# Kernel optimization log

Hardware: AMD Instinct MI355X
Metric: run time of the kernel (lower is better)

Reference implementation:

```python
import jax, jax.numpy as jnp
import numpy as np

D_MODEL = 512
NEG = -1e9


def setup_inputs() -> dict:
    key = jax.random.key(0)
    ks = jax.random.split(key, 8)
    B, S, D = 8, 2048, D_MODEL
    scale = 1.0 / np.sqrt(D)
    x = jax.random.normal(ks[0], (B, S, D), dtype=jnp.float32)
    event_lengths = jax.random.randint(ks[1], (B,), 1, S + 1)
    Wq = jax.random.normal(ks[2], (D, D), dtype=jnp.float32) * scale
    bq = jax.random.normal(ks[3], (D,), dtype=jnp.float32) * 0.01
    Wk = jax.random.normal(ks[4], (D, D), dtype=jnp.float32) * scale
    bk = jax.random.normal(ks[5], (D,), dtype=jnp.float32) * 0.01
    Wv = jax.random.normal(ks[6], (D, D), dtype=jnp.float32) * scale
    bv = jax.random.normal(ks[7], (D,), dtype=jnp.float32) * 0.01
    return {"x": x, "event_lengths": event_lengths, "Wq": Wq, "bq": bq,
            "Wk": Wk, "bk": bk, "Wv": Wv, "bv": bv}


def reference(x, event_lengths, Wq, bq, Wk, bk, Wv, bv):
    B, S, D = x.shape
    inv_scale = 1.0 / jnp.sqrt(jnp.float32(D))
    # torch nn.Linear: y = x @ W^T + b
    q = jnp.einsum('bsd,ed->bse', x, Wq) + bq
    k = jnp.einsum('bsd,ed->bse', x, Wk) + bk
    v = jnp.einsum('bsd,ed->bse', x, Wv) + bv
    scores = jnp.einsum('bqd,bkd->bqk', q, k) * inv_scale  # [B,S,S]
    idx = jnp.arange(S)
    L = event_lengths[:, None, None]  # [B,1,1]
    mask = (idx[None, :, None] < L) & (idx[None, None, :] < L)  # [B,S,S]
    scores = jnp.where(mask, scores, NEG)
    attn = jax.nn.softmax(scores, axis=-1)
    # dropout is identity at eval time
    return jnp.einsum('bqk,bkd->bqd', attn, v)
```

## Files before the change

### kernel.cpp

```cpp
#include <hip/hip_runtime.h>
#include <hip/hip_bf16.h>
#include <cstdint>

#define DEV static __device__ __forceinline__

typedef __attribute__((ext_vector_type(8))) short bf16x8;
typedef __attribute__((ext_vector_type(4))) float f32x4;
typedef __attribute__((ext_vector_type(4))) float float4v;
typedef __attribute__((ext_vector_type(8))) unsigned short us8;
typedef __attribute__((ext_vector_type(4))) unsigned short us4;

constexpr int SEQ = 2048;
constexpr int DM = 512;
constexpr float INV_SCALE = 0.044194173824159216f;
constexpr float LOG2E = 1.4426950408889634f;
constexpr float SEXP = INV_SCALE * LOG2E;

DEV unsigned short f2bf(float f) {
  unsigned int u = __float_as_uint(f);
  u = u + 0x7FFFu + ((u >> 16) & 1u);
  return (unsigned short)(u >> 16);
}
DEV float bf2f(unsigned short h) { return __uint_as_float(((unsigned int)h) << 16); }

DEV void gload_lds16(const void* g, void* l) {
  __builtin_amdgcn_global_load_lds(
      (const __attribute__((address_space(1))) void*)g,
      (__attribute__((address_space(3))) void*)l, 16, 0, 0);
}

__global__ void convert_x_kernel(const float* __restrict__ x, unsigned short* __restrict__ xb) {
  int64_t i = ((int64_t)blockIdx.x * 256 + threadIdx.x) * 8;
  float4v a = *(const float4v*)(x + i);
  float4v b = *(const float4v*)(x + i + 4);
  us8 o;
  o[0] = f2bf(a[0]); o[1] = f2bf(a[1]); o[2] = f2bf(a[2]); o[3] = f2bf(a[3]);
  o[4] = f2bf(b[0]); o[5] = f2bf(b[1]); o[6] = f2bf(b[2]); o[7] = f2bf(b[3]);
  *(us8*)(xb + i) = o;
}

__global__ void convert_w_kernel(const float* __restrict__ wq, const float* __restrict__ wk,
                                 const float* __restrict__ wv, unsigned short* __restrict__ wb) {
  int w = blockIdx.x >> 8;
  int blk = blockIdx.x & 255;
  const float* src = (w == 0) ? wq : ((w == 1) ? wk : wv);
  int i = (blk * 256 + (int)threadIdx.x) * 4;
  float4v a = *(const float4v*)(src + i);
  us4 o;
  o[0] = f2bf(a[0]); o[1] = f2bf(a[1]); o[2] = f2bf(a[2]); o[3] = f2bf(a[3]);
  *(us4*)(wb + (w << 18) + i) = o;
}

__global__ __launch_bounds__(256) void qkv_gemm_kernel(
    const unsigned short* __restrict__ xb, const unsigned short* __restrict__ wb,
    const float* __restrict__ bq, const float* __restrict__ bk, const float* __restrict__ bv,
    const int* __restrict__ ev,
    unsigned short* __restrict__ Qb, unsigned short* __restrict__ Kb,
    unsigned short* __restrict__ VTb)
{
  const int which = blockIdx.z;
  const int m0 = blockIdx.x << 7;
  const int n0 = blockIdx.y << 7;
  if (which < 2) {
    const int L = ev[m0 >> 11];
    if ((m0 & 2047) >= L) return;
  }
  const unsigned short* W = wb + ((int64_t)which << 18);
  const int tid = threadIdx.x;
  const int lane = tid & 63, wid = tid >> 6;
  const int lo = lane & 15, hi = lane >> 4;
  const int wrow = wid >> 1, wcol = wid & 1;

  __shared__ alignas(16) unsigned short lA[128 * 64];
  __shared__ alignas(16) unsigned short lB[128 * 64];

  f32x4 acc[4][4];
  #pragma unroll
  for (int i = 0; i < 4; ++i)
    #pragma unroll
    for (int j = 0; j < 4; ++j) acc[i][j] = (f32x4){0.f, 0.f, 0.f, 0.f};

  for (int k0 = 0; k0 < 512; k0 += 64) {
    if (k0) __syncthreads();
    #pragma unroll
    for (int i = 0; i < 4; ++i) {
      const int m = (i << 8) + tid;
      const int mw = (i << 8) + (wid << 6);
      const int row = m >> 3, c = m & 7;
      const int ca = c ^ (row & 7);
      gload_lds16(xb + ((int64_t)(m0 + row) << 9) + k0 + (ca << 3), lA + (mw << 3));
      gload_lds16(W  + ((int64_t)(n0 + row) << 9) + k0 + (ca << 3), lB + (mw << 3));
    }
    __syncthreads();

    #pragma unroll
    for (int ks = 0; ks < 2; ++ks) {
      bf16x8 af[4], bfr[4];
      #pragma unroll
      for (int mf = 0; mf < 4; ++mf) {
        const int row = (wrow << 6) + (mf << 4) + lo;
        const int cc = ((ks << 2) + hi) ^ (row & 7);
        af[mf] = *(const bf16x8*)(lA + (row << 6) + (cc << 3));
      }
      #pragma unroll
      for (int nf = 0; nf < 4; ++nf) {
        const int row = (wcol << 6) + (nf << 4) + lo;
        const int cc = ((ks << 2) + hi) ^ (row & 7);
        bfr[nf] = *(const bf16x8*)(lB + (row << 6) + (cc << 3));
      }
      #pragma unroll
      for (int mf = 0; mf < 4; ++mf)
        #pragma unroll
        for (int nf = 0; nf < 4; ++nf)
          acc[mf][nf] = __builtin_amdgcn_mfma_f32_16x16x32_bf16(af[mf], bfr[nf], acc[mf][nf], 0, 0, 0);
    }
  }

  const float* bias = (which == 0) ? bq : ((which == 1) ? bk : bv);
  if (which < 2) {
    unsigned short* outp = (which == 0) ? Qb : Kb;
    #pragma unroll
    for (int nf = 0; nf < 4; ++nf) {
      const int e = n0 + (wcol << 6) + (nf << 4) + lo;
      const float bb = bias[e];
      #pragma unroll
      for (int mf = 0; mf < 4; ++mf) {
        const int rowg = m0 + (wrow << 6) + (mf << 4) + (hi << 2);
        #pragma unroll
        for (int r = 0; r < 4; ++r)
          outp[((int64_t)(rowg + r) << 9) + e] = f2bf(acc[mf][nf][r] + bb);
      }
    }
  } else {
    #pragma unroll
    for (int nf = 0; nf < 4; ++nf) {
      const int e = n0 + (wcol << 6) + (nf << 4) + lo;
      const float bb = bias[e];
      #pragma unroll
      for (int mf = 0; mf < 4; ++mf) {
        const int rowg = m0 + (wrow << 6) + (mf << 4) + (hi << 2);
        const int bidx = rowg >> 11;
        const int s = rowg & 2047;
        us4 pk;
        pk[0] = f2bf(acc[mf][nf][0] + bb);
        pk[1] = f2bf(acc[mf][nf][1] + bb);
        pk[2] = f2bf(acc[mf][nf][2] + bb);
        pk[3] = f2bf(acc[mf][nf][3] + bb);
        *(us4*)(VTb + (((int64_t)(bidx << 9) + e) << 11) + s) = pk;
      }
    }
  }
}

__global__ void vmean_kernel(const unsigned short* __restrict__ VTb, float* __restrict__ vmean) {
  const int row = blockIdx.x;
  const unsigned short* src = VTb + (int64_t)row * SEQ;
  const int tid = threadIdx.x;
  us8 v = *(const us8*)(src + tid * 8);
  float s = 0.f;
  #pragma unroll
  for (int j = 0; j < 8; ++j) s += bf2f(v[j]);
  #pragma unroll
  for (int off = 1; off < 64; off <<= 1) s += __shfl_xor(s, off);
  __shared__ float ps[4];
  const int lane = tid & 63, wid = tid >> 6;
  if (lane == 0) ps[wid] = s;
  __syncthreads();
  if (tid == 0) vmean[row] = (ps[0] + ps[1] + ps[2] + ps[3]) * (1.f / 2048.f);
}

__global__ __launch_bounds__(256) void score_gemm_kernel(
    const unsigned short* __restrict__ Qb, const unsigned short* __restrict__ Kb,
    const int* __restrict__ ev, unsigned short* __restrict__ P, int b0)
{
  const int z = blockIdx.z;
  const int b = b0 + z;
  const int L = ev[b];
  const int q0 = blockIdx.x << 7;
  const int k0g = blockIdx.y << 7;
  if (q0 >= L || k0g >= L) return;

  const unsigned short* Qrows = Qb + ((int64_t)b << 20);
  const unsigned short* Krows = Kb + ((int64_t)b << 20);
  const int tid = threadIdx.x;
  const int lane = tid & 63, wid = tid >> 6;
  const int lo = lane & 15, hi = lane >> 4;
  const int wrow = wid >> 1, wcol = wid & 1;

  __shared__ alignas(16) unsigned short lA[128 * 64];
  __shared__ alignas(16) unsigned short lB[128 * 64];

  f32x4 acc[4][4];
  #pragma unroll
  for (int i = 0; i < 4; ++i)
    #pragma unroll
    for (int j = 0; j < 4; ++j) acc[i][j] = (f32x4){0.f, 0.f, 0.f, 0.f};

  for (int k0 = 0; k0 < 512; k0 += 64) {
    if (k0) __syncthreads();
    #pragma unroll
    for (int i = 0; i < 4; ++i) {
      const int m = (i << 8) + tid;
      const int mw = (i << 8) + (wid << 6);
      const int row = m >> 3, c = m & 7;
      const int ca = c ^ (row & 7);
      gload_lds16(Qrows + ((int64_t)(q0 + row) << 9) + k0 + (ca << 3), lA + (mw << 3));
      gload_lds16(Krows + ((int64_t)(k0g + row) << 9) + k0 + (ca << 3), lB + (mw << 3));
    }
    __syncthreads();

    #pragma unroll
    for (int ks = 0; ks < 2; ++ks) {
      bf16x8 af[4], bfr[4];
      #pragma unroll
      for (int mf = 0; mf < 4; ++mf) {
        const int row = (wrow << 6) + (mf << 4) + lo;
        const int cc = ((ks << 2) + hi) ^ (row & 7);
        af[mf] = *(const bf16x8*)(lA + (row << 6) + (cc << 3));
      }
      #pragma unroll
      for (int nf = 0; nf < 4; ++nf) {
        const int row = (wcol << 6) + (nf << 4) + lo;
        const int cc = ((ks << 2) + hi) ^ (row & 7);
        bfr[nf] = *(const bf16x8*)(lB + (row << 6) + (cc << 3));
      }
      #pragma unroll
      for (int mf = 0; mf < 4; ++mf)
        #pragma unroll
        for (int nf = 0; nf < 4; ++nf)
          acc[mf][nf] = __builtin_amdgcn_mfma_f32_16x16x32_bf16(af[mf], bfr[nf], acc[mf][nf], 0, 0, 0);
    }
  }

  unsigned short* Pz = P + ((int64_t)z << 22);
  #pragma unroll
  for (int nf = 0; nf < 4; ++nf) {
    const int kcol = k0g + (wcol << 6) + (nf << 4) + lo;
    const bool kok = kcol < L;
    #pragma unroll
    for (int mf = 0; mf < 4; ++mf) {
      const int rowg = q0 + (wrow << 6) + (mf << 4) + (hi << 2);
      #pragma unroll
      for (int r = 0; r < 4; ++r) {
        const float p = (kok && (rowg + r < L)) ? exp2f(acc[mf][nf][r] * SEXP) : 0.f;
        Pz[((int64_t)(rowg + r) << 11) + kcol] = f2bf(p);
      }
    }
  }
}

__global__ __launch_bounds__(256) void pv_gemm_kernel(
    const unsigned short* __restrict__ P, const unsigned short* __restrict__ VTb,
    const float* __restrict__ vmean, const int* __restrict__ ev,
    float* __restrict__ out, int b0)
{
  const int z = blockIdx.z;
  const int b = b0 + z;
  const int L = ev[b];
  const int q0 = blockIdx.x << 6;
  const int d0 = blockIdx.y << 7;
  const int tid = threadIdx.x;

  float* outb = out + ((int64_t)b << 20);
  const float* vm = vmean + (b << 9);

  if (q0 >= L) {
    #pragma unroll
    for (int j = 0; j < 8; ++j) {
      const int idx = tid + (j << 8);
      const int r = idx >> 5, c = (idx & 31) << 2;
      *(float4v*)(outb + ((int64_t)(q0 + r) << 9) + d0 + c) = *(const float4v*)(vm + d0 + c);
    }
    return;
  }

  const int lane = tid & 63, wid = tid >> 6;
  const int lo = lane & 15, hi = lane >> 4;
  const int wrow = wid >> 1, wcol = wid & 1;

  __shared__ alignas(16) unsigned short lA[2][64 * 64];
  __shared__ alignas(16) unsigned short lB[2][128 * 64];
  __shared__ float lpart[64][4];

  const unsigned short* Pz = P + ((int64_t)z << 22);
  const unsigned short* Vrows = VTb + ((int64_t)(b << 9) << 11);

  f32x4 acc[2][4];
  #pragma unroll
  for (int i = 0; i < 2; ++i)
    #pragma unroll
    for (int j = 0; j < 4; ++j) acc[i][j] = (f32x4){0.f, 0.f, 0.f, 0.f};
  float ls[2] = {0.f, 0.f};

  const int nk = (L + 63) >> 6;

  auto stage = [&](int cur, int kk) {
    #pragma unroll
    for (int i = 0; i < 2; ++i) {
      const int m = (i << 8) + tid;
      const int mw = (i << 8) + (wid << 6);
      const int row = m >> 3, c = m & 7;
      const int ca = c ^ (row & 7);
      gload_lds16(Pz + ((int64_t)(q0 + row) << 11) + (kk << 6) + (ca << 3),
                  &lA[cur][mw << 3]);
    }
    #pragma unroll
    for (int i = 0; i < 4; ++i) {
      const int m = (i << 8) + tid;
      const int mw = (i << 8) + (wid << 6);
      const int row = m >> 3, c = m & 7;
      const int ca = c ^ (row & 7);
      gload_lds16(Vrows + ((int64_t)(d0 + row) << 11) + (kk << 6) + (ca << 3),
                  &lB[cur][mw << 3]);
    }
  };

  stage(0, 0);
  __syncthreads();
  int cur = 0;

  for (int kk = 0; kk < nk; ++kk) {
    if (kk + 1 < nk) stage(cur ^ 1, kk + 1);

    #pragma unroll
    for (int ks = 0; ks < 2; ++ks) {
      bf16x8 af[2], bfr[4];
      #pragma unroll
      for (int mf = 0; mf < 2; ++mf) {
        const int row = (wrow << 5) + (mf << 4) + lo;
        const int cc = ((ks << 2) + hi) ^ (row & 7);
        af[mf] = *(const bf16x8*)(&lA[cur][(row << 6) + (cc << 3)]);
      }
      #pragma unroll
      for (int nf = 0; nf < 4; ++nf) {
        const int row = (wcol << 6) + (nf << 4) + lo;
        const int cc = ((ks << 2) + hi) ^ (row & 7);
        bfr[nf] = *(const bf16x8*)(&lB[cur][(row << 6) + (cc << 3)]);
      }
      if (wcol == 0) {
        #pragma unroll
        for (int mf = 0; mf < 2; ++mf) {
          float t = 0.f;
          #pragma unroll
          for (int j = 0; j < 8; ++j) t += bf2f((unsigned short)af[mf][j]);
          ls[mf] += t;
        }
      }
      #pragma unroll
      for (int mf = 0; mf < 2; ++mf)
        #pragma unroll
        for (int nf = 0; nf < 4; ++nf)
          acc[mf][nf] = __builtin_amdgcn_mfma_f32_16x16x32_bf16(af[mf], bfr[nf], acc[mf][nf], 0, 0, 0);
    }

    __syncthreads();
    cur ^= 1;
  }

  if (wcol == 0) {
    #pragma unroll
    for (int mf = 0; mf < 2; ++mf)
      lpart[(wrow << 5) + (mf << 4) + lo][hi] = ls[mf];
  }
  __syncthreads();

  #pragma unroll
  for (int mf = 0; mf < 2; ++mf) {
    const int rowb = (wrow << 5) + (mf << 4) + (hi << 2);
    float rl[4];
    #pragma unroll
    for (int r = 0; r < 4; ++r) {
      const float l = lpart[rowb + r][0] + lpart[rowb + r][1] +
                      lpart[rowb + r][2] + lpart[rowb + r][3];
      rl[r] = 1.0f / l;
    }
    #pragma unroll
    for (int nf = 0; nf < 4; ++nf) {
      const int col = d0 + (wcol << 6) + (nf << 4) + lo;
      const float vmc = vm[col];
      #pragma unroll
      for (int r = 0; r < 4; ++r) {
        const int rowg = q0 + rowb + r;
        const float val = (rowg < L) ? (acc[mf][nf][r] * rl[r]) : vmc;
        outb[((int64_t)rowg << 9) + col] = val;
      }
    }
  }
}

extern "C" void kernel_launch(void* const* d_in, const int* in_sizes, int n_in,
                              void* d_out, int out_size, void* d_ws, size_t ws_size,
                              hipStream_t stream) {
  const float* x  = (const float*)d_in[0];
  const int* ev   = (const int*)d_in[1];
  const float* Wq = (const float*)d_in[2];
  const float* bq = (const float*)d_in[3];
  const float* Wk = (const float*)d_in[4];
  const float* bk = (const float*)d_in[5];
  const float* Wv = (const float*)d_in[6];
  const float* bv = (const float*)d_in[7];
  float* out = (float*)d_out;

  unsigned short* xb  = (unsigned short*)d_ws;
  unsigned short* wb  = xb + (int64_t)16384 * 512;
  unsigned short* Qb  = wb + 3 * 512 * 512;
  unsigned short* Kb  = Qb + (int64_t)16384 * 512;
  unsigned short* VTb = Kb + (int64_t)16384 * 512;
  float* vmean = (float*)(VTb + (int64_t)16384 * 512);
  unsigned short* Ptail = (unsigned short*)(vmean + 8 * 512);

  const size_t base_bytes = (size_t)((char*)Ptail - (char*)d_ws);
  const size_t pbytes = (size_t)SEQ * SEQ * 2;
  int nb;
  unsigned short* P;
  if (ws_size >= base_bytes + 8 * pbytes)      { nb = 8; P = Ptail; }
  else if (ws_size >= base_bytes + 4 * pbytes) { nb = 4; P = Ptail; }
  else                                         { nb = 2; P = xb; }

  convert_x_kernel<<<4096, 256, 0, stream>>>(x, xb);
  convert_w_kernel<<<768, 256, 0, stream>>>(Wq, Wk, Wv, wb);
  qkv_gemm_kernel<<<dim3(128, 4, 3), 256, 0, stream>>>(xb, wb, bq, bk, bv, ev, Qb, Kb, VTb);
  vmean_kernel<<<4096, 256, 0, stream>>>(VTb, vmean);

  for (int c = 0; c < 8 / nb; ++c) {
    score_gemm_kernel<<<dim3(16, 16, nb), 256, 0, stream>>>(Qb, Kb, ev, P, c * nb);
    pv_gemm_kernel<<<dim3(32, 4, nb), 256, 0, stream>>>(P, VTb, vmean, ev, out, c * nb);
  }
}
```

Baseline: 118.6 us.

## Load P and V fragments directly from global memory, dropping LDS staging

The PV matmul kernel no longer double-buffers P and V tiles in shared memory with async global-to-LDS loads and barriers. Each lane now reads its MFMA fragments straight from global memory. This removes the LDS traffic and the per-iteration __syncthreads, and frees shared memory, which may allow more occupancy. The cost is that there is no explicit prefetch, and each element is reloaded by several waves (P by both column waves, V by both row waves), which relies on cache hits and exposes global latency.

```diff
diff --git a/kernel.cpp b/kernel.cpp
--- a/kernel.cpp
+++ b/kernel.cpp
@@ -278,13 +278,14 @@
   const int lo = lane & 15, hi = lane >> 4;
   const int wrow = wid >> 1, wcol = wid & 1;
 
-  __shared__ alignas(16) unsigned short lA[2][64 * 64];
-  __shared__ alignas(16) unsigned short lB[2][128 * 64];
   __shared__ float lpart[64][4];
 
   const unsigned short* Pz = P + ((int64_t)z << 22);
   const unsigned short* Vrows = VTb + ((int64_t)(b << 9) << 11);
 
+  const unsigned short* pa0 = Pz + ((int64_t)(q0 + (wrow << 5) + lo) << 11) + (hi << 3);
+  const unsigned short* pb0 = Vrows + ((int64_t)(d0 + (wcol << 6) + lo) << 11) + (hi << 3);
+
   f32x4 acc[2][4];
   #pragma unroll
   for (int i = 0; i < 2; ++i)
@@ -293,50 +294,18 @@
   float ls[2] = {0.f, 0.f};
 
   const int nk = (L + 63) >> 6;
-
-  auto stage = [&](int cur, int kk) {
-    #pragma unroll
-    for (int i = 0; i < 2; ++i) {
-      const int m = (i << 8) + tid;
-      const int mw = (i << 8) + (wid << 6);
-      const int row = m >> 3, c = m & 7;
-      const int ca = c ^ (row & 7);
-      gload_lds16(Pz + ((int64_t)(q0 + row) << 11) + (kk << 6) + (ca << 3),
-                  &lA[cur][mw << 3]);
-    }
-    #pragma unroll
-    for (int i = 0; i < 4; ++i) {
-      const int m = (i << 8) + tid;
-      const int mw = (i << 8) + (wid << 6);
-      const int row = m >> 3, c = m & 7;
-      const int ca = c ^ (row & 7);
-      gload_lds16(Vrows + ((int64_t)(d0 + row) << 11) + (kk << 6) + (ca << 3),
-                  &lB[cur][mw << 3]);
-    }
-  };
-
-  stage(0, 0);
-  __syncthreads();
-  int cur = 0;
-
   for (int kk = 0; kk < nk; ++kk) {
-    if (kk + 1 < nk) stage(cur ^ 1, kk + 1);
-
+    const int kb = kk << 6;
     #pragma unroll
     for (int ks = 0; ks < 2; ++ks) {
+      const int ko = kb + (ks << 5);
       bf16x8 af[2], bfr[4];
       #pragma unroll
-      for (int mf = 0; mf < 2; ++mf) {
-        const int row = (wrow << 5) + (mf << 4) + lo;
-        const int cc = ((ks << 2) + hi) ^ (row & 7);
-        af[mf] = *(const bf16x8*)(&lA[cur][(row << 6) + (cc << 3)]);
-      }
-      #pragma unroll
-      for (int nf = 0; nf < 4; ++nf) {
-        const int row = (wcol << 6) + (nf << 4) + lo;
-        const int cc = ((ks << 2) + hi) ^ (row & 7);
-        bfr[nf] = *(const bf16x8*)(&lB[cur][(row << 6) + (cc << 3)]);
-      }
+      for (int mf = 0; mf < 2; ++mf)
+        af[mf] = *(const bf16x8*)(pa0 + ((int64_t)(mf << 4) << 11) + ko);
+      #pragma unroll
+      for (int nf = 0; nf < 4; ++nf)
+        bfr[nf] = *(const bf16x8*)(pb0 + ((int64_t)(nf << 4) << 11) + ko);
       if (wcol == 0) {
         #pragma unroll
         for (int mf = 0; mf < 2; ++mf) {
@@ -352,9 +321,6 @@
         for (int nf = 0; nf < 4; ++nf)
           acc[mf][nf] = __builtin_amdgcn_mfma_f32_16x16x32_bf16(af[mf], bfr[nf], acc[mf][nf], 0, 0, 0);
     }
-
-    __syncthreads();
-    cur ^= 1;
   }
 
   if (wcol == 0) {
```

Result: slower. 183.9 us (+55.1%).
